# Performance work log

Measured on AMD Instinct MI355X. Metric: run time of the kernel, lower is better.

The kernel has to match this reference:

```python
import jax, jax.numpy as jnp
import numpy as np

EPS = 1e-10


def setup_inputs() -> dict:
    key = jax.random.key(0)
    k1, k2 = jax.random.split(key)
    x = jax.random.normal(k1, (64, 512, 256), dtype=jnp.float32)          # (N, code_dim, T)
    codebooks = jax.random.normal(k2, (6, 1024, 512), dtype=jnp.float32)  # (Q, nb_code, code_dim)
    return {"x": x, "codebooks": codebooks}


def _quantize_layer(x_flat, cb):
    # x_flat: (NT, D), cb: (C, D)
    dist = (jnp.sum(x_flat * x_flat, axis=-1, keepdims=True)
            - 2.0 * (x_flat @ cb.T)
            + jnp.sum(cb * cb, axis=-1))          # (NT, C)
    idx = jnp.argmin(dist, axis=-1)               # (NT,)
    x_d = cb[idx]                                 # gather, (NT, D)
    return idx, x_d


def reference(x, codebooks):
    N, D, T = x.shape
    Q, C, _ = codebooks.shape
    NT = N * T

    residual = x
    quantized_out = jnp.zeros_like(x)
    all_indices, losses, perps = [], [], []

    for q in range(Q):  # fixed small number of sequential quantizer stages
        cb = codebooks[q]
        # preprocess: (N, D, T) -> (NT, D)
        x_flat = residual.transpose(0, 2, 1).reshape(NT, D)
        idx, x_d = _quantize_layer(x_flat, cb)

        # commitment loss (codebook side detached; EMA-trained codebook)
        commit_loss = jnp.mean((x_flat - jax.lax.stop_gradient(x_d)) ** 2)

        # perplexity of code usage
        probs = jnp.zeros((C,), dtype=x.dtype).at[idx].add(1.0) / NT
        perplexity = jnp.exp(-jnp.sum(probs * jnp.log(probs + EPS)))

        # straight-through estimator, back to (N, D, T)
        quantized = x_flat + jax.lax.stop_gradient(x_d - x_flat)
        quantized = quantized.reshape(N, T, D).transpose(0, 2, 1)

        residual = residual - jax.lax.stop_gradient(quantized)
        quantized_out = quantized_out + quantized

        all_indices.append(idx.reshape(N, T))
        losses.append(commit_loss)
        perps.append(perplexity)

    all_indices = jnp.stack(all_indices, axis=-1)      # (N, T, Q)
    mean_loss = sum(losses) / Q
    mean_perplexity = sum(perps) / Q
    return quantized_out, all_indices, mean_loss, mean_perplexity
```

## Files before the change

### kernel.cpp

```cpp
#include <hip/hip_runtime.h>
#include <hip/hip_fp16.h>
#include <hip/hip_bf16.h>
#include <stdint.h>


#define NTROWS 16384
#define DDIM   512
#define CCODES 1024
#define QSTAGE 6

#define OFF_R      ((size_t)0)
#define OFF_RBF    ((size_t)33554432)
#define OFF_CBBF   ((size_t)50331648)
#define OFF_CAND   ((size_t)56623104)
#define OFF_CBSQ   ((size_t)58720256)
#define OFF_HIST   ((size_t)58744832)
#define OFF_LOSS   ((size_t)58769408)
#define WS_END     ((size_t)58775552)

#define OUT_IDX_OFF  ((size_t)8388608)
#define OUT_SCAL_OFF ((size_t)8486912)

typedef __attribute__((ext_vector_type(8))) short short8;
typedef __attribute__((ext_vector_type(8))) unsigned short ushort8v;
typedef __attribute__((ext_vector_type(4))) float f32x4;

__device__ __forceinline__ unsigned short f2bf(float f) {
    uint32_t u = __float_as_uint(f);
    uint32_t r = (u + 0x7fffu + ((u >> 16) & 1u)) >> 16;
    return (unsigned short)r;
}
__device__ __forceinline__ uint32_t fkey(float f) {
    uint32_t u = __float_as_uint(f);
    return u ^ ((uint32_t)((int32_t)u >> 31) | 0x80000000u);
}
__device__ __forceinline__ float funkey(uint32_t k) {
    uint32_t u = (k & 0x80000000u) ? (k ^ 0x80000000u) : ~k;
    return __uint_as_float(u);
}
__device__ __forceinline__ uint32_t umin32(uint32_t a, uint32_t b) { return a < b ? a : b; }
__device__ __forceinline__ uint32_t umax32(uint32_t a, uint32_t b) { return a > b ? a : b; }
__device__ __forceinline__ float wave_sum(float v) {
    for (int m = 32; m; m >>= 1) v += __shfl_xor(v, m, 64);
    return v;
}
__device__ __forceinline__ uint32_t wave_min_u32(uint32_t v) {
    for (int m = 32; m; m >>= 1) v = umin32(v, (uint32_t)__shfl_xor((int)v, m, 64));
    return v;
}
__device__ __forceinline__ void async_load16(const void* g, void* l) {
    __builtin_amdgcn_global_load_lds(
        (__attribute__((address_space(1))) void*)(void*)g,
        (__attribute__((address_space(3))) void*)l, 16, 0, 0);
}

__global__ __launch_bounds__(256) void prep_kernel(
    const float* __restrict__ x, const float* __restrict__ cb,
    float* __restrict__ r, unsigned short* __restrict__ rbf,
    unsigned short* __restrict__ cbbf, float* __restrict__ cbsq,
    unsigned int* __restrict__ hist, float* __restrict__ loss_bins)
{
    __shared__ float tile[32][33];
    if (blockIdx.x < 1536) {
        const int wave = threadIdx.x >> 6, lane = threadIdx.x & 63;
        const int row = blockIdx.x * 4 + wave;
        const float* p = cb + (size_t)row * DDIM;
        unsigned short* pb = cbbf + (size_t)row * DDIM;
        float s = 0.f;
#pragma unroll
        for (int t = 0; t < 8; ++t) {
            float v = p[lane + 64 * t];
            pb[lane + 64 * t] = f2bf(v);
            s += v * v;
        }
        s = wave_sum(s);
        if (lane == 0) cbsq[row] = s;
        if (blockIdx.x == 0) {
            for (int i = threadIdx.x; i < QSTAGE * CCODES; i += 256) hist[i] = 0u;
            for (int i = threadIdx.x; i < QSTAGE * 256; i += 256) loss_bins[i] = 0.f;
        }
    } else {
        const int bidx = blockIdx.x - 1536;
        const int d0 = (bidx & 15) * 32;
        const int t0 = ((bidx >> 4) & 7) * 32;
        const int n  = bidx >> 7;
        const int tx = threadIdx.x & 31, ty = threadIdx.x >> 5;
        const float* xp = x + (size_t)n * (DDIM * 256);
#pragma unroll
        for (int s = 0; s < 4; ++s) {
            int dd = ty + s * 8;
            tile[dd][tx] = xp[(size_t)(d0 + dd) * 256 + t0 + tx];
        }
        __syncthreads();
#pragma unroll
        for (int s = 0; s < 4; ++s) {
            int tt = ty + s * 8;
            float v = tile[tx][tt];
            size_t off = (size_t)(n * 256 + t0 + tt) * DDIM + d0 + tx;
            r[off] = v;
            rbf[off] = f2bf(v);
        }
    }
}

#define GBK 32
__global__ __launch_bounds__(512, 2) void gemm_dist_kernel(
    const unsigned short* __restrict__ Abf,
    const unsigned short* __restrict__ Bbf,
    const float* __restrict__ cbsq,
    uint32_t* __restrict__ cand)
{
    __shared__ __align__(16) unsigned short lA[4][256][GBK];
    __shared__ __align__(16) unsigned short lB[4][256][GBK];
    const int tid = threadIdx.x;
    const int wave = tid >> 6, lane = tid & 63;
    const int quad = lane >> 4, l15 = lane & 15;
    const int tm = blockIdx.x, tn = blockIdx.y;
    const int wm = wave >> 2, wn = wave & 3;

    f32x4 acc[8][4];
#pragma unroll
    for (int i = 0; i < 8; ++i)
#pragma unroll
        for (int j = 0; j < 4; ++j) acc[i][j] = (f32x4){0.f, 0.f, 0.f, 0.f};

    const int srow = wave * 32 + (lane >> 2);
    const int gch  = (lane & 3) ^ ((lane >> 3) & 3);
    const unsigned short* gA0 = Abf + ((size_t)tm * 256 + srow) * DDIM + gch * 8;
    const unsigned short* gA1 = gA0 + 16 * DDIM;
    const unsigned short* gB0 = Bbf + ((size_t)tn * 256 + srow) * DDIM + gch * 8;
    const unsigned short* gB1 = gB0 + 16 * DDIM;
    const int dro0 = wave * 32, dro1 = wave * 32 + 16;

#pragma unroll
    for (int st = 0; st < 3; ++st) {
        const size_t ko = (size_t)st * GBK;
        async_load16(gA0 + ko, &lA[st][dro0][0] + lane * 8);
        async_load16(gA1 + ko, &lA[st][dro1][0] + lane * 8);
        async_load16(gB0 + ko, &lB[st][dro0][0] + lane * 8);
        async_load16(gB1 + ko, &lB[st][dro1][0] + lane * 8);
    }
    asm volatile("s_waitcnt vmcnt(8)" ::: "memory");
    __builtin_amdgcn_s_barrier();

    const int cq = (quad ^ ((l15 >> 1) & 3)) * 8;

#pragma unroll
    for (int kt = 0; kt < 16; ++kt) {
        const int buf = kt & 3;
        const int sb  = (kt + 3) & 3;
        const size_t ko = (size_t)(kt + 3) * GBK;

        short8 afA[4], bfr[4];
#pragma unroll
        for (int i = 0; i < 4; ++i)
            afA[i] = *(const short8*)&lA[buf][wm * 128 + i * 16 + l15][cq];
#pragma unroll
        for (int j = 0; j < 4; ++j)
            bfr[j] = *(const short8*)&lB[buf][wn * 64 + j * 16 + l15][cq];
        if (kt <= 12) {
            async_load16(gA0 + ko, &lA[sb][dro0][0] + lane * 8);
            async_load16(gA1 + ko, &lA[sb][dro1][0] + lane * 8);
        }
        __builtin_amdgcn_s_barrier();
        asm volatile("s_waitcnt lgkmcnt(0)" ::: "memory");
        __builtin_amdgcn_sched_barrier(0);
        __builtin_amdgcn_s_setprio(1);
#pragma unroll
        for (int i = 0; i < 4; ++i)
#pragma unroll
            for (int j = 0; j < 4; ++j)
                acc[i][j] = __builtin_amdgcn_mfma_f32_16x16x32_bf16(
                    afA[i], bfr[j], acc[i][j], 0, 0, 0);
        __builtin_amdgcn_s_setprio(0);
        __builtin_amdgcn_s_barrier();

        short8 afB[4];
#pragma unroll
        for (int i = 0; i < 4; ++i)
            afB[i] = *(const short8*)&lA[buf][wm * 128 + (i + 4) * 16 + l15][cq];
        if (kt <= 12) {
            async_load16(gB0 + ko, &lB[sb][dro0][0] + lane * 8);
            async_load16(gB1 + ko, &lB[sb][dro1][0] + lane * 8);
        }
        __builtin_amdgcn_s_barrier();
        asm volatile("s_waitcnt lgkmcnt(0)" ::: "memory");
        __builtin_amdgcn_sched_barrier(0);
        __builtin_amdgcn_s_setprio(1);
#pragma unroll
        for (int i = 0; i < 4; ++i)
#pragma unroll
            for (int j = 0; j < 4; ++j)
                acc[i + 4][j] = __builtin_amdgcn_mfma_f32_16x16x32_bf16(
                    afB[i], bfr[j], acc[i + 4][j], 0, 0, 0);
        __builtin_amdgcn_s_setprio(0);

        if (kt <= 12)      asm volatile("s_waitcnt vmcnt(8)" ::: "memory");
        else if (kt == 13) asm volatile("s_waitcnt vmcnt(4)" ::: "memory");
        else if (kt == 14) asm volatile("s_waitcnt vmcnt(0)" ::: "memory");
        if (kt < 15) __builtin_amdgcn_s_barrier();
    }

    const int rowq = tm * 256 + wm * 128 + quad * 4;
    const int colb = tn * 256 + wn * 64 + l15;
    const int g    = tn * 4 + wn;
    float cbs[4];
#pragma unroll
    for (int j = 0; j < 4; ++j) cbs[j] = cbsq[colb + j * 16];
#pragma unroll
    for (int i = 0; i < 8; ++i) {
#pragma unroll
        for (int reg = 0; reg < 4; ++reg) {
            const int row = rowq + i * 16 + reg;
            uint32_t k[4];
#pragma unroll
            for (int j = 0; j < 4; ++j) {
                float dv = cbs[j] - 2.0f * acc[i][j][reg];
                k[j] = (fkey(dv) & ~1023u) | (uint32_t)(colb + j * 16);
            }
            uint32_t m01 = umin32(k[0], k[1]), M01 = umax32(k[0], k[1]);
            uint32_t m23 = umin32(k[2], k[3]), M23 = umax32(k[2], k[3]);
            uint32_t k1 = umin32(m01, m23);
            uint32_t k2 = umin32(umax32(m01, m23), umin32(M01, M23));
#pragma unroll
            for (int m = 1; m < 16; m <<= 1) {
                uint32_t o1 = (uint32_t)__shfl_xor((int)k1, m, 64);
                uint32_t o2 = (uint32_t)__shfl_xor((int)k2, m, 64);
                uint32_t n1 = umin32(k1, o1);
                uint32_t n2 = umin32(umax32(k1, o1), umin32(k2, o2));
                k1 = n1; k2 = n2;
            }
            if (l15 == 0)
                *(uint2*)&cand[((size_t)row * 16 + g) * 2] = make_uint2(k1, k2);
        }
    }
}

#define MARGIN 8.0f
__global__ __launch_bounds__(256) void refine_kernel(
    float* __restrict__ r, unsigned short* __restrict__ rbf,
    const float* __restrict__ cbq, const float* __restrict__ cbsqq,
    const uint32_t* __restrict__ cand,
    float* __restrict__ out_idx, unsigned int* __restrict__ histq,
    float* __restrict__ loss_bins, int q, int write_bf)
{
    const int wave = threadIdx.x >> 6, lane = threadIdx.x & 63;
    const int nt = blockIdx.x * 4 + wave;

    const float4* r4 = (const float4*)(r + (size_t)nt * DDIM);
    float4 ra = r4[lane * 2], rb = r4[lane * 2 + 1];
    float s = ra.x * ra.x + ra.y * ra.y + ra.z * ra.z + ra.w * ra.w
            + rb.x * rb.x + rb.y * rb.y + rb.z * rb.z + rb.w * rb.w;
    const float sumx = wave_sum(s);

    uint32_t key = 0xFFFFFFFFu;
    if (lane < 32) key = cand[(size_t)nt * 32 + lane];
    const uint32_t kmin = wave_min_u32(key);
    const float thr = funkey(kmin & ~1023u) + MARGIN;

    unsigned long long mask = __ballot(lane < 32 && funkey(key & ~1023u) <= thr);

    float best = 1e30f;
    int bestc = CCODES;
    while (mask) {
        const int src = __ffsll(mask) - 1;
        mask &= mask - 1;
        const int cc = __shfl((int)(key & 1023u), src, 64);
        const float4* crow = (const float4*)(cbq + (size_t)cc * DDIM);
        float4 ca = crow[lane * 2], cb2 = crow[lane * 2 + 1];
        float dot = ra.x * ca.x + ra.y * ca.y + ra.z * ca.z + ra.w * ca.w
                  + rb.x * cb2.x + rb.y * cb2.y + rb.z * cb2.z + rb.w * cb2.w;
        dot = wave_sum(dot);
        const float de = (sumx - 2.0f * dot) + cbsqq[cc];
        if (de < best || (de == best && cc < bestc)) { best = de; bestc = cc; }
    }

    const float4* cbest = (const float4*)(cbq + (size_t)bestc * DDIM);
    float4 ba = cbest[lane * 2], bb = cbest[lane * 2 + 1];
    float4 na = make_float4(ra.x - ba.x, ra.y - ba.y, ra.z - ba.z, ra.w - ba.w);
    float4 nb = make_float4(rb.x - bb.x, rb.y - bb.y, rb.z - bb.z, rb.w - bb.w);
    float4* rw = (float4*)(r + (size_t)nt * DDIM);
    rw[lane * 2] = na; rw[lane * 2 + 1] = nb;
    if (write_bf) {
        ushort8v pk;
        pk[0] = f2bf(na.x); pk[1] = f2bf(na.y); pk[2] = f2bf(na.z); pk[3] = f2bf(na.w);
        pk[4] = f2bf(nb.x); pk[5] = f2bf(nb.y); pk[6] = f2bf(nb.z); pk[7] = f2bf(nb.w);
        *(ushort8v*)(rbf + (size_t)nt * DDIM + lane * 8) = pk;
    }

    if (lane == 0) {
        out_idx[(size_t)nt * QSTAGE + q] = (float)bestc;
        atomicAdd(&histq[bestc], 1u);
        atomicAdd(&loss_bins[q * 256 + (blockIdx.x & 255)], best);
    }
}

__global__ __launch_bounds__(256) void final_kernel(
    const float* __restrict__ x, const float* __restrict__ r,
    float* __restrict__ out,
    const unsigned int* __restrict__ hist, const float* __restrict__ loss_bins,
    float* __restrict__ out2)
{
    __shared__ float tile[32][33];
    __shared__ float red[4];
    __shared__ float perp_acc;
    const int tid = threadIdx.x, wave = tid >> 6, lane = tid & 63;

    if (blockIdx.x < 8192) {
        const int bidx = blockIdx.x;
        const int d0 = (bidx & 15) * 32;
        const int t0 = ((bidx >> 4) & 7) * 32;
        const int n  = bidx >> 7;
        const int tx = tid & 31, ty = tid >> 5;
#pragma unroll
        for (int s = 0; s < 4; ++s) {
            int tt = ty + s * 8;
            tile[tt][tx] = r[(size_t)(n * 256 + t0 + tt) * DDIM + d0 + tx];
        }
        __syncthreads();
        const float* xp = x + (size_t)n * (DDIM * 256);
        float* op = out + (size_t)n * (DDIM * 256);
#pragma unroll
        for (int s = 0; s < 4; ++s) {
            int dd = ty + s * 8;
            size_t off = (size_t)(d0 + dd) * 256 + t0 + tx;
            op[off] = xp[off] - tile[tx][dd];
        }
        return;
    }

    if (tid == 0) perp_acc = 0.f;
    __syncthreads();
    for (int q = 0; q < QSTAGE; ++q) {
        float s = 0.f;
        for (int c = tid; c < CCODES; c += 256) {
            float p = (float)hist[q * CCODES + c] * (1.0f / (float)NTROWS);
            s += p * logf(p + 1e-10f);
        }
        s = wave_sum(s);
        if (lane == 0) red[wave] = s;
        __syncthreads();
        if (tid == 0) {
            float tot = red[0] + red[1] + red[2] + red[3];
            perp_acc += expf(-tot);
        }
        __syncthreads();
    }
    float ls = 0.f;
    for (int i = tid; i < QSTAGE * 256; i += 256) ls += loss_bins[i];
    ls = wave_sum(ls);
    if (lane == 0) red[wave] = ls;
    __syncthreads();
    if (tid == 0) {
        float lsum = red[0] + red[1] + red[2] + red[3];
        out2[0] = (lsum / (float)QSTAGE) / ((float)NTROWS * (float)DDIM);
        out2[1] = perp_acc / (float)QSTAGE;
    }
}

extern "C" void kernel_launch(void* const* d_in, const int* in_sizes, int n_in,
                              void* d_out, int out_size, void* d_ws, size_t ws_size,
                              hipStream_t stream)
{
    const float* x  = (const float*)d_in[0];
    const float* cb = (const float*)d_in[1];
    float* out = (float*)d_out;
    char* ws = (char*)d_ws;

    float*          r      = (float*)(ws + OFF_R);
    unsigned short* rbf    = (unsigned short*)(ws + OFF_RBF);
    unsigned short* cbbf   = (unsigned short*)(ws + OFF_CBBF);
    uint32_t*       cand   = (uint32_t*)(ws + OFF_CAND);
    float*          cbsq   = (float*)(ws + OFF_CBSQ);
    unsigned int*   hist   = (unsigned int*)(ws + OFF_HIST);
    float*          lbins  = (float*)(ws + OFF_LOSS);

    prep_kernel<<<9728, 256, 0, stream>>>(x, cb, r, rbf, cbbf, cbsq, hist, lbins);

    for (int q = 0; q < QSTAGE; ++q) {
        const size_t cboff = (size_t)q * CCODES * DDIM;
        gemm_dist_kernel<<<dim3(64, 4), 512, 0, stream>>>(
            rbf, cbbf + cboff, cbsq + q * CCODES, cand);
        refine_kernel<<<4096, 256, 0, stream>>>(
            r, rbf, cb + cboff, cbsq + q * CCODES, cand,
            out + OUT_IDX_OFF, hist + q * CCODES, lbins,
            q, (q < QSTAGE - 1) ? 1 : 0);
    }

    final_kernel<<<8193, 256, 0, stream>>>(x, r, out, hist, lbins,
                                           out + OUT_SCAL_OFF);
}
```

Before: 471.0 us.

## Split refine candidates across four waves per row with shared-memory argmin

The refine kernel now gives each row its own 256-thread block instead of one wave, and the row's surviving candidate codes are dealt round-robin to the four waves. Each wave computes exact distances for its share, and the per-wave minima are packed into 64-bit keys and reduced through shared memory. The residual update and bf16 write are then spread over all 256 threads. This shortens the serial per-row candidate loop and raises parallelism, at the cost of four times as many blocks, redundant residual and norm loads in every wave, and a block barrier.

Measured after the change: 453.9 us. 1.04x faster.

```diff
diff --git a/kernel.cpp b/kernel.cpp
--- a/kernel.cpp
+++ b/kernel.cpp
@@ -40,6 +40,10 @@
 }
 __device__ __forceinline__ uint32_t umin32(uint32_t a, uint32_t b) { return a < b ? a : b; }
 __device__ __forceinline__ uint32_t umax32(uint32_t a, uint32_t b) { return a > b ? a : b; }
+__device__ __forceinline__ unsigned long long umin64(unsigned long long a,
+                                                     unsigned long long b) {
+    return a < b ? a : b;
+}
 __device__ __forceinline__ float wave_sum(float v) {
     for (int m = 32; m; m >>= 1) v += __shfl_xor(v, m, 64);
     return v;
@@ -244,8 +248,13 @@
     float* __restrict__ out_idx, unsigned int* __restrict__ histq,
     float* __restrict__ loss_bins, int q, int write_bf)
 {
-    const int wave = threadIdx.x >> 6, lane = threadIdx.x & 63;
-    const int nt = blockIdx.x * 4 + wave;
+    __shared__ unsigned long long sbest[4];
+    const int tid = threadIdx.x;
+    const int wave = tid >> 6, lane = tid & 63;
+    const int nt = blockIdx.x;
+
+    uint32_t key = 0xFFFFFFFFu;
+    if (lane < 32) key = cand[(size_t)nt * 32 + lane];
 
     const float4* r4 = (const float4*)(r + (size_t)nt * DDIM);
     float4 ra = r4[lane * 2], rb = r4[lane * 2 + 1];
@@ -253,18 +262,17 @@
             + rb.x * rb.x + rb.y * rb.y + rb.z * rb.z + rb.w * rb.w;
     const float sumx = wave_sum(s);
 
-    uint32_t key = 0xFFFFFFFFu;
-    if (lane < 32) key = cand[(size_t)nt * 32 + lane];
     const uint32_t kmin = wave_min_u32(key);
     const float thr = funkey(kmin & ~1023u) + MARGIN;
-
     unsigned long long mask = __ballot(lane < 32 && funkey(key & ~1023u) <= thr);
 
     float best = 1e30f;
     int bestc = CCODES;
+    int cnt = 0;
     while (mask) {
         const int src = __ffsll(mask) - 1;
         mask &= mask - 1;
+        if ((cnt++ & 3) != wave) continue;
         const int cc = __shfl((int)(key & 1023u), src, 64);
         const float4* crow = (const float4*)(cbq + (size_t)cc * DDIM);
         float4 ca = crow[lane * 2], cb2 = crow[lane * 2 + 1];
@@ -274,21 +282,25 @@
         const float de = (sumx - 2.0f * dot) + cbsqq[cc];
         if (de < best || (de == best && cc < bestc)) { best = de; bestc = cc; }
     }
-
-    const float4* cbest = (const float4*)(cbq + (size_t)bestc * DDIM);
-    float4 ba = cbest[lane * 2], bb = cbest[lane * 2 + 1];
-    float4 na = make_float4(ra.x - ba.x, ra.y - ba.y, ra.z - ba.z, ra.w - ba.w);
-    float4 nb = make_float4(rb.x - bb.x, rb.y - bb.y, rb.z - bb.z, rb.w - bb.w);
-    float4* rw = (float4*)(r + (size_t)nt * DDIM);
-    rw[lane * 2] = na; rw[lane * 2 + 1] = nb;
+    if (lane == 0)
+        sbest[wave] = ((unsigned long long)fkey(best) << 32) | (unsigned)bestc;
+    __syncthreads();
+    const unsigned long long bmin =
+        umin64(umin64(sbest[0], sbest[1]), umin64(sbest[2], sbest[3]));
+    bestc = (int)(bmin & 0xFFFFFFFFu);
+    best  = funkey((uint32_t)(bmin >> 32));
+
+    const float2* rr  = (const float2*)(r + (size_t)nt * DDIM);
+    const float2* cbr = (const float2*)(cbq + (size_t)bestc * DDIM);
+    float2 rv = rr[tid], cv = cbr[tid];
+    float2 nv = make_float2(rv.x - cv.x, rv.y - cv.y);
+    ((float2*)(r + (size_t)nt * DDIM))[tid] = nv;
     if (write_bf) {
-        ushort8v pk;
-        pk[0] = f2bf(na.x); pk[1] = f2bf(na.y); pk[2] = f2bf(na.z); pk[3] = f2bf(na.w);
-        pk[4] = f2bf(nb.x); pk[5] = f2bf(nb.y); pk[6] = f2bf(nb.z); pk[7] = f2bf(nb.w);
-        *(ushort8v*)(rbf + (size_t)nt * DDIM + lane * 8) = pk;
-    }
-
-    if (lane == 0) {
+        uint32_t pk = (uint32_t)f2bf(nv.x) | ((uint32_t)f2bf(nv.y) << 16);
+        ((uint32_t*)(rbf + (size_t)nt * DDIM))[tid] = pk;
+    }
+
+    if (tid == 0) {
         out_idx[(size_t)nt * QSTAGE + q] = (float)bestc;
         atomicAdd(&histq[bestc], 1u);
         atomicAdd(&loss_bins[q * 256 + (blockIdx.x & 255)], best);
@@ -381,7 +393,7 @@
         const size_t cboff = (size_t)q * CCODES * DDIM;
         gemm_dist_kernel<<<dim3(64, 4), 512, 0, stream>>>(
             rbf, cbbf + cboff, cbsq + q * CCODES, cand);
-        refine_kernel<<<4096, 256, 0, stream>>>(
+        refine_kernel<<<NTROWS, 256, 0, stream>>>(
             r, rbf, cb + cboff, cbsq + q * CCODES, cand,
             out + OUT_IDX_OFF, hist + q * CCODES, lbins,
             q, (q < QSTAGE - 1) ? 1 : 0);
```

## Evaluate eight refine candidates per pass using 8-lane groups and LDS row

Applied to the files above, without the earlier changes.

The refine kernel no longer walks surviving candidates one at a time with a full-wave dot product and a 6-step reduction each. It stores the residual row in swizzled LDS and splits the wave into eight 8-lane groups, each computing one candidate's dot product with a 3-step shuffle reduction. The best candidate is picked through a packed 64-bit (distance key, index) min reduction, and ||x||^2 is only added after selection. This cuts serialized shuffle reductions and raises memory-level parallelism on codebook loads, at the cost of LDS traffic, a serial loop to find each group's mask bit, and slightly different float summation order in the distance.

After: 562.3 us. +19.4%, slower.

```diff
diff --git a/kernel.cpp b/kernel.cpp
--- a/kernel.cpp
+++ b/kernel.cpp
@@ -40,6 +40,10 @@
 }
 __device__ __forceinline__ uint32_t umin32(uint32_t a, uint32_t b) { return a < b ? a : b; }
 __device__ __forceinline__ uint32_t umax32(uint32_t a, uint32_t b) { return a > b ? a : b; }
+__device__ __forceinline__ unsigned long long umin64(unsigned long long a,
+                                                     unsigned long long b) {
+    return a < b ? a : b;
+}
 __device__ __forceinline__ float wave_sum(float v) {
     for (int m = 32; m; m >>= 1) v += __shfl_xor(v, m, 64);
     return v;
@@ -47,6 +51,12 @@
 __device__ __forceinline__ uint32_t wave_min_u32(uint32_t v) {
     for (int m = 32; m; m >>= 1) v = umin32(v, (uint32_t)__shfl_xor((int)v, m, 64));
     return v;
+}
+__device__ __forceinline__ unsigned long long shflx64(unsigned long long v, int m) {
+    uint32_t lo = (uint32_t)v, hi = (uint32_t)(v >> 32);
+    lo = (uint32_t)__shfl_xor((int)lo, m, 64);
+    hi = (uint32_t)__shfl_xor((int)hi, m, 64);
+    return ((unsigned long long)hi << 32) | lo;
 }
 __device__ __forceinline__ void async_load16(const void* g, void* l) {
     __builtin_amdgcn_global_load_lds(
@@ -244,54 +254,86 @@
     float* __restrict__ out_idx, unsigned int* __restrict__ histq,
     float* __restrict__ loss_bins, int q, int write_bf)
 {
+    __shared__ float rowbuf[4][512];
     const int wave = threadIdx.x >> 6, lane = threadIdx.x & 63;
     const int nt = blockIdx.x * 4 + wave;
+    const int s = lane & 7;
 
     const float4* r4 = (const float4*)(r + (size_t)nt * DDIM);
     float4 ra = r4[lane * 2], rb = r4[lane * 2 + 1];
-    float s = ra.x * ra.x + ra.y * ra.y + ra.z * ra.z + ra.w * ra.w
-            + rb.x * rb.x + rb.y * rb.y + rb.z * rb.z + rb.w * rb.w;
-    const float sumx = wave_sum(s);
-
     uint32_t key = 0xFFFFFFFFu;
     if (lane < 32) key = cand[(size_t)nt * 32 + lane];
-    const uint32_t kmin = wave_min_u32(key);
-    const float thr = funkey(kmin & ~1023u) + MARGIN;
-
+
+    {
+        const int j0 = lane * 2, j1 = lane * 2 + 1;
+        float4* rbv = (float4*)rowbuf[wave];
+        rbv[j0 ^ ((j0 >> 4) & 7)] = ra;
+        rbv[j1 ^ ((j1 >> 4) & 7)] = rb;
+    }
+
+    const uint32_t kminw = wave_min_u32(key);
+    const float thr = funkey(kminw & ~1023u) + MARGIN;
     unsigned long long mask = __ballot(lane < 32 && funkey(key & ~1023u) <= thr);
-
-    float best = 1e30f;
-    int bestc = CCODES;
-    while (mask) {
-        const int src = __ffsll(mask) - 1;
-        mask &= mask - 1;
+    const int nsurv = (int)__popcll(mask);
+    const int npass = (nsurv + 7) >> 3;
+
+    unsigned long long bestpk = ~0ull;
+    for (int p = 0; p < npass; ++p) {
+        const int myidx = p * 8 + (lane >> 3);
+        const bool active = myidx < nsurv;
+        unsigned long long mm = mask;
+        for (int t = 0; t < myidx; ++t) mm &= mm - 1;
+        int src = active ? (__ffsll(mm) - 1) : 0;
         const int cc = __shfl((int)(key & 1023u), src, 64);
-        const float4* crow = (const float4*)(cbq + (size_t)cc * DDIM);
-        float4 ca = crow[lane * 2], cb2 = crow[lane * 2 + 1];
-        float dot = ra.x * ca.x + ra.y * ca.y + ra.z * ca.z + ra.w * ca.w
-                  + rb.x * cb2.x + rb.y * cb2.y + rb.z * cb2.z + rb.w * cb2.w;
-        dot = wave_sum(dot);
-        const float de = (sumx - 2.0f * dot) + cbsqq[cc];
-        if (de < best || (de == best && cc < bestc)) { best = de; bestc = cc; }
-    }
+
+        const float4* crow = (const float4*)(cbq + (size_t)cc * DDIM + s * 64);
+        const float4* rbv = (const float4*)rowbuf[wave];
+        float ax = 0.f, ay = 0.f, az = 0.f, aw = 0.f;
+#pragma unroll
+        for (int k = 0; k < 16; ++k) {
+            const float4 cv = crow[k];
+            const int j = s * 16 + k;
+            const float4 rv = rbv[j ^ ((j >> 4) & 7)];
+            ax += rv.x * cv.x; ay += rv.y * cv.y;
+            az += rv.z * cv.z; aw += rv.w * cv.w;
+        }
+        float d = (ax + ay) + (az + aw);
+        d += __shfl_xor(d, 1, 64);
+        d += __shfl_xor(d, 2, 64);
+        d += __shfl_xor(d, 4, 64);
+        unsigned long long pk = ~0ull;
+        if (active) {
+            const float part = cbsqq[cc] - 2.0f * d;
+            pk = (((unsigned long long)fkey(part)) << 32) | (unsigned)cc;
+        }
+        pk = umin64(pk, shflx64(pk, 8));
+        pk = umin64(pk, shflx64(pk, 16));
+        pk = umin64(pk, shflx64(pk, 32));
+        bestpk = umin64(bestpk, pk);
+    }
+    const int bestc = (int)(uint32_t)bestpk;
+    const float bpart = funkey((uint32_t)(bestpk >> 32));
 
     const float4* cbest = (const float4*)(cbq + (size_t)bestc * DDIM);
     float4 ba = cbest[lane * 2], bb = cbest[lane * 2 + 1];
+    float sq = ra.x * ra.x + ra.y * ra.y + ra.z * ra.z + ra.w * ra.w
+             + rb.x * rb.x + rb.y * rb.y + rb.z * rb.z + rb.w * rb.w;
+    const float sumx = wave_sum(sq);
     float4 na = make_float4(ra.x - ba.x, ra.y - ba.y, ra.z - ba.z, ra.w - ba.w);
     float4 nb = make_float4(rb.x - bb.x, rb.y - bb.y, rb.z - bb.z, rb.w - bb.w);
     float4* rw = (float4*)(r + (size_t)nt * DDIM);
     rw[lane * 2] = na; rw[lane * 2 + 1] = nb;
     if (write_bf) {
-        ushort8v pk;
-        pk[0] = f2bf(na.x); pk[1] = f2bf(na.y); pk[2] = f2bf(na.z); pk[3] = f2bf(na.w);
-        pk[4] = f2bf(nb.x); pk[5] = f2bf(nb.y); pk[6] = f2bf(nb.z); pk[7] = f2bf(nb.w);
-        *(ushort8v*)(rbf + (size_t)nt * DDIM + lane * 8) = pk;
+        ushort8v pk8;
+        pk8[0] = f2bf(na.x); pk8[1] = f2bf(na.y); pk8[2] = f2bf(na.z); pk8[3] = f2bf(na.w);
+        pk8[4] = f2bf(nb.x); pk8[5] = f2bf(nb.y); pk8[6] = f2bf(nb.z); pk8[7] = f2bf(nb.w);
+        *(ushort8v*)(rbf + (size_t)nt * DDIM + lane * 8) = pk8;
     }
 
     if (lane == 0) {
         out_idx[(size_t)nt * QSTAGE + q] = (float)bestc;
         atomicAdd(&histq[bestc], 1u);
-        atomicAdd(&loss_bins[q * 256 + (blockIdx.x & 255)], best);
+        atomicAdd(&loss_bins[q * 256 + (nt & 255)], sumx + bpart);
     }
 }
 
```
